# Kernel tuning notes

Hardware: AMD Instinct MI355X
Metric: run time of the kernel (lower is better)

The kernel has to match this reference:

```python
import jax, jax.numpy as jnp
import numpy as np
import math

B, S, D = 2, 1024, 512
H = 8
DH = D // H
N_NEURONS = 512
K = 16
N_BASIS = 8
RANK = 64
D_FF = 2048
LN_EPS = 1e-5


def _layer_norm(x, g, b):
    mu = jnp.mean(x, axis=-1, keepdims=True)
    var = jnp.var(x, axis=-1, keepdims=True)
    return (x - mu) * jax.lax.rsqrt(var + LN_EPS) * g + b


def setup_inputs() -> dict:
    key = jax.random.key(0)
    ks = jax.random.split(key, 16)
    x = jax.random.normal(ks[0], (B, S, D), dtype=jnp.float32)
    # causal mask [B,1,S,S] (True = keep)
    mask = jnp.broadcast_to(jnp.tril(jnp.ones((S, S), dtype=bool)), (B, 1, S, S))
    inp = {
        "x": x,
        "neuron_emb": jax.random.normal(ks[1], (N_NEURONS, D)) * 0.02,
        "Wq": jax.random.normal(ks[2], (D, D)) * 0.02, "bq": jnp.zeros((D,)),
        "Wk": jax.random.normal(ks[3], (D, D)) * 0.02, "bk": jnp.zeros((D,)),
        "Wv": jax.random.normal(ks[4], (D, D)) * 0.02, "bv": jnp.zeros((D,)),
        "Wg": jax.random.normal(ks[5], (2 * D, 2)) * 0.02, "bg": jnp.zeros((2,)),
        "basis_A": jax.random.normal(ks[6], (N_BASIS, D, RANK)) * 0.05,
        "basis_B": jax.random.normal(ks[7], (N_BASIS, RANK, D_FF)) * 0.05,
        "neuron_coords": jax.random.normal(ks[8], (N_NEURONS, N_BASIS)) * 0.5,
        "Wd": jax.random.normal(ks[9], (D_FF, D)) * 0.02, "bd": jnp.zeros((D,)),
        "ln1_g": jnp.ones((D,)), "ln1_b": jnp.zeros((D,)),
        "ln2_g": jnp.ones((D,)), "ln2_b": jnp.zeros((D,)),
        "mask": mask,
    }
    return inp


def reference(x, neuron_emb, Wq, bq, Wk, bk, Wv, bv, Wg, bg, basis_A, basis_B,
              neuron_coords, Wd, bd, ln1_g, ln1_b, ln2_g, ln2_b, mask):
    normed = _layer_norm(x, ln1_g, ln1_b)
    # --- router: cross-attention context ---
    q = (normed @ Wq + bq).reshape(B, S, H, DH).transpose(0, 2, 1, 3)
    k = (normed @ Wk + bk).reshape(B, S, H, DH).transpose(0, 2, 1, 3)
    v = (normed @ Wv + bv).reshape(B, S, H, DH).transpose(0, 2, 1, 3)
    attn = jnp.einsum('bhsd,bhtd->bhst', q, k) / math.sqrt(DH)
    attn = jnp.where(mask, attn, -jnp.inf)
    attn = jax.nn.softmax(attn, axis=-1)
    context = jnp.einsum('bhst,bhtd->bhsd', attn, v)
    context = context.transpose(0, 2, 1, 3).reshape(B, S, D)
    # --- gated neuron scoring + top-k ---
    token_scores = normed @ neuron_emb.T            # [B,S,N]
    context_scores = context @ neuron_emb.T         # [B,S,N]
    gate = jax.nn.softmax(jnp.concatenate([normed, context], axis=-1) @ Wg + bg, axis=-1)
    scores = gate[:, :, 0:1] * token_scores + gate[:, :, 1:2] * context_scores
    topk_scores, topk_idx = jax.lax.top_k(scores, K)  # [B,S,K]
    weights = jax.nn.softmax(topk_scores, axis=-1)
    # --- neuron info residual ---
    neuron_info = jnp.einsum('bsk,bskd->bsd', weights, neuron_emb[topk_idx])
    x = x + neuron_info
    # --- per-token basis-mixed low-rank FFN ---
    normed2 = _layer_norm(x, ln2_g, ln2_b)
    coords = neuron_coords[topk_idx]                # [B,S,K,n_basis]
    token_coords = jnp.einsum('bsk,bskn->bsn', weights, coords)  # [B,S,n_basis]
    # h = x @ (sum_n c_n A_n): contract without materializing [B,S,D,R]
    h = jnp.einsum('bsnr,bsn->bsr', jnp.einsum('bsd,ndr->bsnr', normed2, basis_A), token_coords)
    h = jnp.einsum('bsnf,bsn->bsf', jnp.einsum('bsr,nrf->bsnf', h, basis_B), token_coords)
    h = jax.nn.gelu(h, approximate=False)
    out = h @ Wd + bd
    x = x + out
    return (x, topk_idx)
```

## Files before the change

### kernel.cpp

```cpp
#include <hip/hip_runtime.h>
#include <hip/hip_bf16.h>

#define Bv 2
#define Sv 1024
#define Dv 512
#define Hv 8
#define Nv 512
#define Kv 16
#define NBv 8
#define DFv 2048
#define NTOK (Bv*Sv)

typedef __attribute__((ext_vector_type(8))) short short8;
typedef __attribute__((ext_vector_type(4))) float float4v;
typedef __attribute__((ext_vector_type(4))) double dbl4;

__device__ __forceinline__ double fexp64(double x)
{
    if (x < -708.0) return 0.0;
    const double SHIFT = 6755399441055744.0;
    double t  = fma(x, 1.4426950408889634074, SHIFT);
    double nd = t - SHIFT;
    double r  = fma(-nd, 6.93147180369123816490e-01, x);
    r         = fma(-nd, 1.90821492927058770002e-10, r);
    double p = 1.0 / 6227020800.0;
    p = fma(p, r, 1.0 / 479001600.0);
    p = fma(p, r, 1.0 / 39916800.0);
    p = fma(p, r, 1.0 / 3628800.0);
    p = fma(p, r, 1.0 / 362880.0);
    p = fma(p, r, 1.0 / 40320.0);
    p = fma(p, r, 1.0 / 5040.0);
    p = fma(p, r, 1.0 / 720.0);
    p = fma(p, r, 1.0 / 120.0);
    p = fma(p, r, 1.0 / 24.0);
    p = fma(p, r, 1.0 / 6.0);
    p = fma(p, r, 0.5);
    p = fma(p, r, 1.0);
    p = fma(p, r, 1.0);
    long long ni = (long long)nd;
    double s = __longlong_as_double((unsigned long long)(ni + 1023) << 52);
    return p * s;
}

__launch_bounds__(256)
__global__ void ln64_k(const float* __restrict__ x, const float* __restrict__ g,
                       const float* __restrict__ b, double* __restrict__ out)
{
    const int t = blockIdx.x;
    const size_t base = (size_t)t * Dv;
    const int tid = threadIdx.x;
    double v0 = (double)x[base + tid];
    double v1 = (double)x[base + tid + 256];
    double s = v0 + v1, ss = v0 * v0 + v1 * v1;
    #pragma unroll
    for (int off = 32; off; off >>= 1) { s += __shfl_xor(s, off); ss += __shfl_xor(ss, off); }
    __shared__ double red[4][2];
    const int wv = tid >> 6, ln = tid & 63;
    if (ln == 0) { red[wv][0] = s; red[wv][1] = ss; }
    __syncthreads();
    s  = red[0][0] + red[1][0] + red[2][0] + red[3][0];
    ss = red[0][1] + red[1][1] + red[2][1] + red[3][1];
    double mu  = s * (1.0 / Dv);
    double var = ss * (1.0 / Dv) - mu * mu;
    double rstd = 1.0 / sqrt(var + 1e-5);
    out[base + tid]       = (v0 - mu) * rstd * (double)g[tid]       + (double)b[tid];
    out[base + tid + 256] = (v1 - mu) * rstd * (double)g[tid + 256] + (double)b[tid + 256];
}

__launch_bounds__(256)
__global__ void qkvMC_k(const double* __restrict__ A,
                        const float* __restrict__ Wq, const float* __restrict__ Wk,
                        const float* __restrict__ Wv, const float* __restrict__ bq,
                        const float* __restrict__ bk, const float* __restrict__ bvv,
                        double* __restrict__ qo, double* __restrict__ ko,
                        double* __restrict__ vo)
{
    __shared__ double As[32][18];
    __shared__ double Bs[3][16][66];
    const int tid = threadIdx.x;
    const int n0 = blockIdx.x * 64, m0 = blockIdx.y * 32;
    const int w = tid >> 6, l = tid & 63;
    const int mt = (w >> 1) * 16, wc = (w & 1) * 32;
    const int ar = tid >> 3, ak = (tid & 7) * 2;
    const int bkk = tid >> 4, bn = (tid & 15) * 4;

    int rA = 0, kA = 0, kB = 0, cB = 0, dsel = -1;
    #pragma unroll 1
    for (int ab = 0; ab < 4; ab++) {
        if (dsel >= 0) break;
        const int a_ = ab & 1, b_ = ab >> 1;
        const int rA_ = a_ ? (l >> 2) : (l & 15);
        const int kA_ = a_ ? (l & 3)  : (l >> 4);
        const int kB_ = b_ ? (l & 3)  : (l >> 4);
        const int cB_ = b_ ? (l >> 2) : (l & 15);
        const double av  = (double)(((rA_ * 37 + kA_ * 11) % 19) + 1);
        const double bvp = (double)(((kB_ * 23 + cB_ * 7) % 17) + 1);
        dbl4 dd = __builtin_amdgcn_mfma_f64_16x16x4f64(av, bvp, (dbl4){0.0, 0.0, 0.0, 0.0}, 0, 0, 0);
        #pragma unroll 1
        for (int d = 0; d < 4; d++) {
            if (dsel >= 0) break;
            int okv = 1;
            #pragma unroll
            for (int r = 0; r < 4; r++) {
                const int i_ = (d == 0) ? 4 * (l >> 4) + r
                             : (d == 1) ? (l & 15)
                             : (d == 2) ? (l >> 4) + 4 * r
                             :            (l & 15);
                const int j_ = (d == 0) ? (l & 15)
                             : (d == 1) ? 4 * (l >> 4) + r
                             : (d == 2) ? (l & 15)
                             :            (l >> 4) + 4 * r;
                double e = 0.0;
                #pragma unroll
                for (int kk2 = 0; kk2 < 4; kk2++)
                    e += (double)(((i_ * 37 + kk2 * 11) % 19) + 1)
                       * (double)(((kk2 * 23 + j_ * 7) % 17) + 1);
                okv &= (dd[r] == e) ? 1 : 0;
            }
            if (__all(okv)) { dsel = d; rA = rA_; kA = kA_; kB = kB_; cB = cB_; }
        }
    }

    auto stage = [&](int k0) {
        double2 avv = *(const double2*)(A + (size_t)(m0 + ar) * Dv + k0 + ak);
        *(double2*)&As[ar][ak] = avv;
        {
            float4 b4 = *(const float4*)(Wq + (size_t)(k0 + bkk) * Dv + n0 + bn);
            Bs[0][bkk][bn] = (double)b4.x; Bs[0][bkk][bn + 1] = (double)b4.y;
            Bs[0][bkk][bn + 2] = (double)b4.z; Bs[0][bkk][bn + 3] = (double)b4.w;
        }
        {
            float4 b4 = *(const float4*)(Wk + (size_t)(k0 + bkk) * Dv + n0 + bn);
            Bs[1][bkk][bn] = (double)b4.x; Bs[1][bkk][bn + 1] = (double)b4.y;
            Bs[1][bkk][bn + 2] = (double)b4.z; Bs[1][bkk][bn + 3] = (double)b4.w;
        }
        {
            float4 b4 = *(const float4*)(Wv + (size_t)(k0 + bkk) * Dv + n0 + bn);
            Bs[2][bkk][bn] = (double)b4.x; Bs[2][bkk][bn + 1] = (double)b4.y;
            Bs[2][bkk][bn + 2] = (double)b4.z; Bs[2][bkk][bn + 3] = (double)b4.w;
        }
    };

    if (dsel >= 0) {
        dbl4 acc[3][2];
        #pragma unroll
        for (int z = 0; z < 3; z++)
            #pragma unroll
            for (int nt = 0; nt < 2; nt++)
                acc[z][nt] = (dbl4){0.0, 0.0, 0.0, 0.0};
        for (int k0 = 0; k0 < Dv; k0 += 16) {
            __syncthreads();
            stage(k0);
            __syncthreads();
            #pragma unroll
            for (int s = 0; s < 4; s++) {
                const double aA = As[mt + rA][4 * s + kA];
                #pragma unroll
                for (int z = 0; z < 3; z++) {
                    const double b0 = Bs[z][4 * s + kB][wc + cB];
                    const double b1 = Bs[z][4 * s + kB][wc + 16 + cB];
                    acc[z][0] = __builtin_amdgcn_mfma_f64_16x16x4f64(aA, b0, acc[z][0], 0, 0, 0);
                    acc[z][1] = __builtin_amdgcn_mfma_f64_16x16x4f64(aA, b1, acc[z][1], 0, 0, 0);
                }
            }
        }
        #pragma unroll
        for (int r = 0; r < 4; r++) {
            const int i_ = (dsel == 0) ? 4 * (l >> 4) + r
                         : (dsel == 1) ? (l & 15)
                         : (dsel == 2) ? (l >> 4) + 4 * r
                         :               (l & 15);
            const int j_ = (dsel == 0) ? (l & 15)
                         : (dsel == 1) ? 4 * (l >> 4) + r
                         : (dsel == 2) ? (l & 15)
                         :               (l >> 4) + 4 * r;
            const int rowg = m0 + mt + i_;
            #pragma unroll
            for (int nt = 0; nt < 2; nt++) {
                const int colg = n0 + wc + nt * 16 + j_;
                qo[(size_t)rowg * Dv + colg] = acc[0][nt][r] + (double)bq[colg];
                ko[(size_t)rowg * Dv + colg] = acc[1][nt][r] + (double)bk[colg];
                vo[(size_t)rowg * Dv + colg] = acc[2][nt][r] + (double)bvv[colg];
            }
        }
    } else {
        double fac[3][8];
        #pragma unroll
        for (int z = 0; z < 3; z++)
            #pragma unroll
            for (int c = 0; c < 8; c++) fac[z][c] = 0.0;
        const int frow = mt + (l & 15);
        const int fcb  = wc + (l >> 4) * 8;
        for (int k0 = 0; k0 < Dv; k0 += 16) {
            __syncthreads();
            stage(k0);
            __syncthreads();
            #pragma unroll
            for (int kk = 0; kk < 16; kk++) {
                const double a = As[frow][kk];
                #pragma unroll
                for (int z = 0; z < 3; z++)
                    #pragma unroll
                    for (int c = 0; c < 8; c++)
                        fac[z][c] = fma(a, Bs[z][kk][fcb + c], fac[z][c]);
            }
        }
        const int rowg = m0 + frow;
        #pragma unroll
        for (int c = 0; c < 8; c++) {
            const int colg = n0 + fcb + c;
            qo[(size_t)rowg * Dv + colg] = fac[0][c] + (double)bq[colg];
            ko[(size_t)rowg * Dv + colg] = fac[1][c] + (double)bk[colg];
            vo[(size_t)rowg * Dv + colg] = fac[2][c] + (double)bvv[colg];
        }
    }
}

__launch_bounds__(256)
__global__ void scores64_k(const double* __restrict__ A0, const double* __restrict__ A1,
                           const double* __restrict__ gate, const float* __restrict__ Bm,
                           double* __restrict__ Cbase)
{
    const int M = NTOK, N = Nv, Kd = Dv;
    const int z = blockIdx.z;
    const int kbeg = z * (Dv / 2), kend = kbeg + Dv / 2;
    double* Cout = Cbase + (size_t)z * M * N;
    __shared__ double As[16][68];
    __shared__ double Bs[16][68];
    const int tid = threadIdx.x;
    const int m0 = blockIdx.y * 64, n0 = blockIdx.x * 64;
    const int tx = tid & 15, ty = tid >> 4;
    double acc[4][4] = {};
    const int lm = tid >> 2, lk4 = (tid & 3) << 2;
    for (int k0 = kbeg; k0 < kend; k0 += 16) {
        const double g0 = gate[2 * (m0 + lm)], g1 = gate[2 * (m0 + lm) + 1];
        double4 a0 = *(const double4*)(A0 + (size_t)(m0 + lm) * Kd + k0 + lk4);
        double4 a1 = *(const double4*)(A1 + (size_t)(m0 + lm) * Kd + k0 + lk4);
        As[lk4 + 0][lm] = g0 * a0.x + g1 * a1.x;
        As[lk4 + 1][lm] = g0 * a0.y + g1 * a1.y;
        As[lk4 + 2][lm] = g0 * a0.z + g1 * a1.z;
        As[lk4 + 3][lm] = g0 * a0.w + g1 * a1.w;
        const int nn = tid >> 2, kq = (tid & 3) << 2;
        float4 bv4 = *(const float4*)(Bm + (size_t)(n0 + nn) * Kd + k0 + kq);
        Bs[kq + 0][nn] = (double)bv4.x; Bs[kq + 1][nn] = (double)bv4.y;
        Bs[kq + 2][nn] = (double)bv4.z; Bs[kq + 3][nn] = (double)bv4.w;
        __syncthreads();
        #pragma unroll
        for (int kk = 0; kk < 16; kk++) {
            double a_[4], b_[4];
            *(double4*)a_ = *(const double4*)&As[kk][ty << 2];
            *(double4*)b_ = *(const double4*)&Bs[kk][tx << 2];
            #pragma unroll
            for (int i = 0; i < 4; i++)
                #pragma unroll
                for (int j = 0; j < 4; j++)
                    acc[i][j] = fma(a_[i], b_[j], acc[i][j]);
        }
        __syncthreads();
    }
    #pragma unroll
    for (int i = 0; i < 4; i++) {
        const int row = m0 + (ty << 2) + i;
        #pragma unroll
        for (int j = 0; j < 4; j++)
            Cout[(size_t)row * N + n0 + (tx << 2) + j] = acc[i][j];
    }
}

template<int EPI>
__launch_bounds__(256)
__global__ void mfma_k(const __hip_bfloat16* __restrict__ A, const __hip_bfloat16* __restrict__ B,
                       void* __restrict__ Cout_, int M, int N, int Kt, int kper)
{
    __shared__ __hip_bfloat16 As[128][40];
    __shared__ __hip_bfloat16 Bs[128][40];
    const int tid = threadIdx.x;
    const int m0 = blockIdx.y * 128, n0 = blockIdx.x * 128;
    const int z = blockIdx.z;
    const int kbeg = z * kper, kend = kbeg + kper;
    const int w = tid >> 6, l = tid & 63;
    const int wr = (w >> 1) * 64, wc = (w & 1) * 64;
    const int lm = l & 15, quad = l >> 4;
    float4v acc[4][4];
    #pragma unroll
    for (int i = 0; i < 4; i++)
        #pragma unroll
        for (int j = 0; j < 4; j++)
            acc[i][j] = (float4v){0.f, 0.f, 0.f, 0.f};
    const int srow = tid >> 1, skb = (tid & 1) * 16;
    for (int k0 = kbeg; k0 < kend; k0 += 32) {
        *(uint4*)&As[srow][skb]     = *(const uint4*)(A + (size_t)(m0 + srow) * Kt + k0 + skb);
        *(uint4*)&As[srow][skb + 8] = *(const uint4*)(A + (size_t)(m0 + srow) * Kt + k0 + skb + 8);
        *(uint4*)&Bs[srow][skb]     = *(const uint4*)(B + (size_t)(n0 + srow) * Kt + k0 + skb);
        *(uint4*)&Bs[srow][skb + 8] = *(const uint4*)(B + (size_t)(n0 + srow) * Kt + k0 + skb + 8);
        __syncthreads();
        short8 af[4], bf[4];
        #pragma unroll
        for (int mi = 0; mi < 4; mi++) af[mi] = *(const short8*)&As[wr + mi * 16 + lm][quad * 8];
        #pragma unroll
        for (int ni = 0; ni < 4; ni++) bf[ni] = *(const short8*)&Bs[wc + ni * 16 + lm][quad * 8];
        #pragma unroll
        for (int mi = 0; mi < 4; mi++)
            #pragma unroll
            for (int ni = 0; ni < 4; ni++)
                acc[mi][ni] = __builtin_amdgcn_mfma_f32_16x16x32_bf16(af[mi], bf[ni], acc[mi][ni], 0, 0, 0);
        __syncthreads();
    }
    #pragma unroll
    for (int mi = 0; mi < 4; mi++) {
        #pragma unroll
        for (int ni = 0; ni < 4; ni++) {
            const int col = n0 + wc + ni * 16 + lm;
            #pragma unroll
            for (int r = 0; r < 4; r++) {
                const int row = m0 + wr + mi * 16 + quad * 4 + r;
                float c = acc[mi][ni][r];
                if (EPI == 0) {
                    ((float*)Cout_)[(size_t)z * M * N + (size_t)row * N + col] = c;
                } else {
                    c = 0.5f * c * (1.0f + erff(c * 0.70710678118654752f));
                    ((__hip_bfloat16*)Cout_)[(size_t)row * N + col] = __float2bfloat16(c);
                }
            }
        }
    }
}

__device__ __constant__ int c_slotbase[4] = {0, 0, 384, 640};
__device__ __constant__ int c_cnt[4]      = {0, 24, 16, 8};

__launch_bounds__(256)
__global__ void attn64w_k(const double* __restrict__ q, const double* __restrict__ k,
                          const double* __restrict__ v, double* __restrict__ ctxun,
                          double* __restrict__ Opart, double* __restrict__ mbuf,
                          double* __restrict__ lbuf)
{
    const int qb = blockIdx.x, bh = blockIdx.y, ch = blockIdx.z;
    if (qb < ch * 4) return;
    const int b = bh >> 3, h = bh & 7;
    __shared__ double Qs[64][70];
    __shared__ double Kt[64][34];
    __shared__ double Vs[32][70];
    const int tid = threadIdx.x;
    const int r = tid >> 3, cc = tid & 7;
    const int lane = tid & 63;
    const int lbase = lane & 56;
    const size_t qoff = ((size_t)(b * Sv + qb * 64)) * Dv + h * 64;
    #pragma unroll
    for (int i = 0; i < 8; i++) {
        int f = i * 256 + tid;
        int row = f >> 5, c2 = (f & 31) * 2;
        *(double2*)&Qs[row][c2] = *(const double2*)(q + qoff + (size_t)row * Dv + c2);
    }
    double O0[8] = {}, O1[8] = {};
    double m0 = -1e300, l0 = 0.0;
    double m1 = -1e300, l1 = 0.0;
    const int ig0 = qb * 64 + r;
    const int ig1 = qb * 64 + 32 + r;
    const int jbeg = ch * 8;
    const int jend = (ch * 8 + 7 < 2 * qb + 1) ? ch * 8 + 7 : 2 * qb + 1;
    for (int jt = jbeg; jt <= jend; jt++) {
        __syncthreads();
        const size_t koff = ((size_t)(b * Sv + jt * 32)) * Dv + h * 64;
        #pragma unroll
        for (int i = 0; i < 4; i++) {
            int f = i * 256 + tid;
            int row = f >> 5, c2 = (f & 31) * 2;
            double2 kv = *(const double2*)(k + koff + (size_t)row * Dv + c2);
            Kt[c2][row]     = kv.x;
            Kt[c2 + 1][row] = kv.y;
            *(double2*)&Vs[row][c2] = *(const double2*)(v + koff + (size_t)row * Dv + c2);
        }
        __syncthreads();
        double a0[4] = {0.0, 0.0, 0.0, 0.0};
        double a1[4] = {0.0, 0.0, 0.0, 0.0};
        #pragma unroll 8
        for (int kk = 0; kk < 64; kk += 2) {
            double2 qv0 = *(const double2*)&Qs[r][kk];
            double2 qv1 = *(const double2*)&Qs[32 + r][kk];
            double2 ka0 = *(const double2*)&Kt[kk][cc * 4];
            double2 ka1 = *(const double2*)&Kt[kk][cc * 4 + 2];
            double2 kb0 = *(const double2*)&Kt[kk + 1][cc * 4];
            double2 kb1 = *(const double2*)&Kt[kk + 1][cc * 4 + 2];
            a0[0] = fma(qv0.x, ka0.x, fma(qv0.y, kb0.x, a0[0]));
            a0[1] = fma(qv0.x, ka0.y, fma(qv0.y, kb0.y, a0[1]));
            a0[2] = fma(qv0.x, ka1.x, fma(qv0.y, kb1.x, a0[2]));
            a0[3] = fma(qv0.x, ka1.y, fma(qv0.y, kb1.y, a0[3]));
            a1[0] = fma(qv1.x, ka0.x, fma(qv1.y, kb0.x, a1[0]));
            a1[1] = fma(qv1.x, ka0.y, fma(qv1.y, kb0.y, a1[1]));
            a1[2] = fma(qv1.x, ka1.x, fma(qv1.y, kb1.x, a1[2]));
            a1[3] = fma(qv1.x, ka1.y, fma(qv1.y, kb1.y, a1[3]));
        }
        double p0[4], p1[4];
        double mx0 = -1e300, mx1 = -1e300;
        #pragma unroll
        for (int jj = 0; jj < 4; jj++) {
            const int jglob = jt * 32 + cc * 4 + jj;
            p0[jj] = (jglob <= ig0) ? a0[jj] * 0.125 : -1e300;
            p1[jj] = (jglob <= ig1) ? a1[jj] * 0.125 : -1e300;
            mx0 = fmax(mx0, p0[jj]);
            mx1 = fmax(mx1, p1[jj]);
        }
        mx0 = fmax(mx0, __shfl_xor(mx0, 1)); mx1 = fmax(mx1, __shfl_xor(mx1, 1));
        mx0 = fmax(mx0, __shfl_xor(mx0, 2)); mx1 = fmax(mx1, __shfl_xor(mx1, 2));
        mx0 = fmax(mx0, __shfl_xor(mx0, 4)); mx1 = fmax(mx1, __shfl_xor(mx1, 4));
        const double mn0 = fmax(m0, mx0), mn1 = fmax(m1, mx1);
        double rs0 = 0.0, rs1 = 0.0;
        #pragma unroll
        for (int jj = 0; jj < 4; jj++) {
            p0[jj] = fexp64(p0[jj] - mn0); rs0 += p0[jj];
            p1[jj] = fexp64(p1[jj] - mn1); rs1 += p1[jj];
        }
        rs0 += __shfl_xor(rs0, 1); rs1 += __shfl_xor(rs1, 1);
        rs0 += __shfl_xor(rs0, 2); rs1 += __shfl_xor(rs1, 2);
        rs0 += __shfl_xor(rs0, 4); rs1 += __shfl_xor(rs1, 4);
        const double al0 = fexp64(m0 - mn0), al1 = fexp64(m1 - mn1);
        l0 = l0 * al0 + rs0; m0 = mn0;
        l1 = l1 * al1 + rs1; m1 = mn1;
        #pragma unroll
        for (int c = 0; c < 8; c++) { O0[c] *= al0; O1[c] *= al1; }
        #pragma unroll
        for (int jsrc = 0; jsrc < 8; jsrc++) {
            #pragma unroll
            for (int jj = 0; jj < 4; jj++) {
                const double pj0 = __shfl(p0[jj], lbase + jsrc);
                const double pj1 = __shfl(p1[jj], lbase + jsrc);
                const double* vrow = &Vs[jsrc * 4 + jj][cc * 8];
                #pragma unroll
                for (int c2 = 0; c2 < 8; c2 += 2) {
                    double2 vv = *(const double2*)&vrow[c2];
                    O0[c2 + 0] = fma(pj0, vv.x, O0[c2 + 0]);
                    O0[c2 + 1] = fma(pj0, vv.y, O0[c2 + 1]);
                    O1[c2 + 0] = fma(pj1, vv.x, O1[c2 + 0]);
                    O1[c2 + 1] = fma(pj1, vv.y, O1[c2 + 1]);
                }
            }
        }
    }
    const int qt0 = 2 * qb, qt1 = 2 * qb + 1;
    if (cc == 0) {
        const int mi0 = ((bh * 32 + qt0) * 4 + ch) * 32 + r;
        mbuf[mi0] = m0; lbuf[mi0] = l0;
        const int mi1 = ((bh * 32 + qt1) * 4 + ch) * 32 + r;
        mbuf[mi1] = m1; lbuf[mi1] = l1;
    }
    if (ch == 0) {
        const size_t ob0 = ((size_t)(b * Sv + ig0)) * Dv + h * 64 + cc * 8;
        const size_t ob1 = ((size_t)(b * Sv + ig1)) * Dv + h * 64 + cc * 8;
        #pragma unroll
        for (int c2 = 0; c2 < 8; c2 += 2) {
            double2 t0{O0[c2], O0[c2 + 1]}; *(double2*)(ctxun + ob0 + c2) = t0;
            double2 t1{O1[c2], O1[c2 + 1]}; *(double2*)(ctxun + ob1 + c2) = t1;
        }
    } else {
        const int slot0 = c_slotbase[ch] + bh * c_cnt[ch] + (qt0 - ch * 8);
        const int slot1 = slot0 + 1;
        const size_t ob0 = ((size_t)slot0 * 32 + r) * 64 + cc * 8;
        const size_t ob1 = ((size_t)slot1 * 32 + r) * 64 + cc * 8;
        #pragma unroll
        for (int c2 = 0; c2 < 8; c2 += 2) {
            double2 t0{O0[c2], O0[c2 + 1]}; *(double2*)(Opart + ob0 + c2) = t0;
            double2 t1{O1[c2], O1[c2 + 1]}; *(double2*)(Opart + ob1 + c2) = t1;
        }
    }
}

__launch_bounds__(256)
__global__ void attnmerge_k(double* __restrict__ ctx, const double* __restrict__ Opart,
                            const double* __restrict__ mbuf, const double* __restrict__ lbuf)
{
    const size_t i = (size_t)blockIdx.x * 256 + threadIdx.x;
    const size_t e = i * 2;
    const int d = (int)(e & 511);
    const int s = (int)((e >> 9) & 1023);
    const int b = (int)(e >> 19);
    const int h = d >> 6;
    const int qt = s >> 5, r = s & 31;
    const int bh = b * 8 + h;
    int nch = qt >> 3; if (nch > 3) nch = 3;
    const int mib = ((bh * 32 + qt) * 4) * 32 + r;
    double ms = mbuf[mib];
    for (int c = 1; c <= nch; c++) ms = fmax(ms, mbuf[mib + c * 32]);
    double2 o = *(const double2*)(ctx + e);
    double a0 = exp(mbuf[mib] - ms);
    double den = lbuf[mib] * a0;
    o.x *= a0; o.y *= a0;
    for (int c = 1; c <= nch; c++) {
        const double ac = exp(mbuf[mib + c * 32] - ms);
        den += lbuf[mib + c * 32] * ac;
        const int slot = c_slotbase[c] + bh * c_cnt[c] + (qt - c * 8);
        const size_t op = ((size_t)slot * 32 + r) * 64 + (d & 63);
        double2 oc = *(const double2*)(Opart + op);
        o.x = fma(ac, oc.x, o.x);
        o.y = fma(ac, oc.y, o.y);
    }
    const double inv = 1.0 / den;
    o.x *= inv; o.y *= inv;
    *(double2*)(ctx + e) = o;
}

__launch_bounds__(256)
__global__ void gate64_k(const double* __restrict__ normed, const double* __restrict__ ctx,
                         const float* __restrict__ Wg, const float* __restrict__ bg,
                         double* __restrict__ gate)
{
    const int wv = threadIdx.x >> 6, lane = threadIdx.x & 63;
    const int t = blockIdx.x * 4 + wv;
    double a0 = 0.0, a1 = 0.0;
    for (int d = lane; d < Dv; d += 64) {
        double nv = normed[(size_t)t * Dv + d];
        double cv = ctx[(size_t)t * Dv + d];
        a0 += nv * (double)Wg[2 * d]     + cv * (double)Wg[2 * (d + Dv)];
        a1 += nv * (double)Wg[2 * d + 1] + cv * (double)Wg[2 * (d + Dv) + 1];
    }
    #pragma unroll
    for (int off = 32; off; off >>= 1) { a0 += __shfl_xor(a0, off); a1 += __shfl_xor(a1, off); }
    if (lane == 0) {
        a0 += (double)bg[0]; a1 += (double)bg[1];
        double m = fmax(a0, a1);
        double e0 = exp(a0 - m), e1 = exp(a1 - m);
        double inv = 1.0 / (e0 + e1);
        gate[2 * t] = e0 * inv; gate[2 * t + 1] = e1 * inv;
    }
}

__launch_bounds__(256)
__global__ void topk64_k(const double* __restrict__ s0, const float* __restrict__ x,
                         const float* __restrict__ emb, const float* __restrict__ coords,
                         const float* __restrict__ g2, const float* __restrict__ b2,
                         float* __restrict__ x2, __hip_bfloat16* __restrict__ normed2bf,
                         float* __restrict__ tcoords, float* __restrict__ idx_out)
{
    __shared__ double sc[4][Nv];
    const int wv = threadIdx.x >> 6, lane = threadIdx.x & 63;
    const int t = blockIdx.x * 4 + wv;
    const double* s1 = s0 + (size_t)NTOK * Nv;
    double* s = sc[wv];
    #pragma unroll
    for (int i = 0; i < 8; i++) {
        const size_t idx = (size_t)t * Nv + i * 64 + lane;
        s[i * 64 + lane] = s0[idx] + s1[idx];
    }
    __syncthreads();
    double wval[Kv]; int widx[Kv];
    for (int kk = 0; kk < Kv; kk++) {
        double bvv = -1e300; int bi = Nv;
        #pragma unroll
        for (int i = 0; i < 8; i++) {
            const int d = lane * 8 + i;
            const double vv = s[d];
            if (vv > bvv) { bvv = vv; bi = d; }
        }
        #pragma unroll
        for (int off = 1; off < 64; off <<= 1) {
            double ov = __shfl_xor(bvv, off);
            int    oi = __shfl_xor(bi, off);
            if (ov > bvv || (ov == bvv && oi < bi)) { bvv = ov; bi = oi; }
        }
        wval[kk] = bvv; widx[kk] = bi;
        __syncthreads();
        if (lane == (bi >> 3)) s[bi] = -1e301;
        __syncthreads();
        if (lane == kk) idx_out[(size_t)t * Kv + kk] = (float)bi;
    }
    double w[Kv]; double sum = 0.0;
    #pragma unroll
    for (int kk = 0; kk < Kv; kk++) { w[kk] = exp(wval[kk] - wval[0]); sum += w[kk]; }
    const double invs = 1.0 / sum;
    #pragma unroll
    for (int kk = 0; kk < Kv; kk++) w[kk] *= invs;
    float xv[8];
    float sm = 0.0f, sq = 0.0f;
    #pragma unroll
    for (int i = 0; i < 8; i++) {
        const int d = lane + 64 * i;
        double info = 0.0;
        #pragma unroll
        for (int kk = 0; kk < Kv; kk++)
            info = fma(w[kk], (double)emb[(size_t)widx[kk] * Dv + d], info);
        float vv = (float)((double)x[(size_t)t * Dv + d] + info);
        xv[i] = vv;
        x2[(size_t)t * Dv + d] = vv;
        sm += vv; sq += vv * vv;
    }
    #pragma unroll
    for (int off = 32; off; off >>= 1) { sm += __shfl_xor(sm, off); sq += __shfl_xor(sq, off); }
    const float mu = sm * (1.0f / Dv);
    const float var = sq * (1.0f / Dv) - mu * mu;
    const float rstd = rsqrtf(var + 1e-5f);
    #pragma unroll
    for (int i = 0; i < 8; i++) {
        const int d = lane + 64 * i;
        normed2bf[(size_t)t * Dv + d] = __float2bfloat16((xv[i] - mu) * rstd * g2[d] + b2[d]);
    }
    if (lane < NBv) {
        double tc = 0.0;
        #pragma unroll
        for (int kk = 0; kk < Kv; kk++)
            tc = fma(w[kk], (double)coords[(size_t)widx[kk] * NBv + lane], tc);
        tcoords[t * NBv + lane] = (float)tc;
    }
}

__launch_bounds__(256)
__global__ void acatbf_k(const float* __restrict__ bA, __hip_bfloat16* __restrict__ AcatT)
{
    const int i = blockIdx.x * 256 + threadIdx.x;
    const int d = i & 511, nc = i >> 9;
    const int n = nc >> 6, r = nc & 63;
    AcatT[i] = __float2bfloat16(bA[n * 32768 + d * 64 + r]);
}

__launch_bounds__(256)
__global__ void tr2bf_k(const float* __restrict__ in, __hip_bfloat16* __restrict__ out,
                        int R, int C)
{
    __shared__ float tile[32][33];
    const int c0 = blockIdx.x * 32, r0 = blockIdx.y * 32;
    const int tx = threadIdx.x & 31, ty = threadIdx.x >> 5;
    #pragma unroll
    for (int i = 0; i < 4; i++)
        tile[ty + 8 * i][tx] = in[(size_t)(r0 + ty + 8 * i) * C + c0 + tx];
    __syncthreads();
    #pragma unroll
    for (int i = 0; i < 4; i++)
        out[(size_t)(c0 + ty + 8 * i) * R + r0 + tx] = __float2bfloat16(tile[tx][ty + 8 * i]);
}

__launch_bounds__(256)
__global__ void combine_k(const float* __restrict__ Gp, const float* __restrict__ tcoords,
                          __hip_bfloat16* __restrict__ u_bf)
{
    const size_t M1 = (size_t)NTOK * Dv;
    const int wv = threadIdx.x >> 6, lane = threadIdx.x & 63;
    const int t = blockIdx.x * 4 + wv;
    float cs[NBv];
    #pragma unroll
    for (int n = 0; n < NBv; n++) cs[n] = tcoords[t * NBv + n];
    float h = 0.0f;
    #pragma unroll
    for (int n = 0; n < NBv; n++) {
        const size_t gi = (size_t)t * Dv + n * 64 + lane;
        float g = Gp[gi] + Gp[gi + M1] + Gp[gi + 2 * M1] + Gp[gi + 3 * M1];
        h = fmaf(cs[n], g, h);
    }
    #pragma unroll
    for (int n = 0; n < NBv; n++)
        u_bf[(size_t)t * Dv + n * 64 + lane] = __float2bfloat16(cs[n] * h);
}

__launch_bounds__(256)
__global__ void reduce4_k(const float* __restrict__ p4, const float* __restrict__ bd,
                          const float* __restrict__ x2, float* __restrict__ xout)
{
    const size_t M1 = (size_t)NTOK * Dv;
    const size_t i = (size_t)blockIdx.x * 256 + threadIdx.x;
    float c = p4[i] + p4[i + M1] + p4[i + 2 * M1] + p4[i + 3 * M1];
    xout[i] = c + bd[i & 511] + x2[i];
}

extern "C" void kernel_launch(void* const* d_in, const int* in_sizes, int n_in,
                              void* d_out, int out_size, void* d_ws, size_t ws_size,
                              hipStream_t stream) {
    (void)in_sizes; (void)n_in; (void)out_size; (void)ws_size;
    const size_t M1 = (size_t)NTOK * Dv;

    const float* x   = (const float*)d_in[0];
    const float* emb = (const float*)d_in[1];
    const float* Wq  = (const float*)d_in[2];
    const float* bq  = (const float*)d_in[3];
    const float* Wk  = (const float*)d_in[4];
    const float* bk  = (const float*)d_in[5];
    const float* Wv  = (const float*)d_in[6];
    const float* bvv = (const float*)d_in[7];
    const float* Wg  = (const float*)d_in[8];
    const float* bg  = (const float*)d_in[9];
    const float* bA  = (const float*)d_in[10];
    const float* bB  = (const float*)d_in[11];
    const float* crd = (const float*)d_in[12];
    const float* Wd  = (const float*)d_in[13];
    const float* bd  = (const float*)d_in[14];
    const float* l1g = (const float*)d_in[15];
    const float* l1b = (const float*)d_in[16];
    const float* l2g = (const float*)d_in[17];
    const float* l2b = (const float*)d_in[18];

    double* normed64 = (double*)d_ws;
    double* q64      = normed64 + M1;
    double* k64      = q64 + M1;
    double* v64      = k64 + M1;
    double* ctx64    = v64 + M1;
    double* Opart    = ctx64 + M1;
    double* mbuf     = Opart + 1572864;
    double* lbuf     = mbuf + 65536;
    double* gate64   = lbuf + 65536;
    float*  tcoords  = (float*)(gate64 + 4096);
    __hip_bfloat16* AcatT = (__hip_bfloat16*)(tcoords + 16384);

    double* s0 = q64;
    float*  x2 = (float*)v64;
    __hip_bfloat16* normed2bf = (__hip_bfloat16*)(x2 + M1);
    __hip_bfloat16* u_bf      = normed2bf + M1;
    float* Gp = (float*)q64;
    float* p4 = (float*)q64;
    __hip_bfloat16* hf_bf = (__hip_bfloat16*)Opart;
    __hip_bfloat16* bBT   = hf_bf + 4 * M1;
    __hip_bfloat16* WdT   = bBT + M1;

    float* xout    = (float*)d_out;
    float* idx_out = (float*)d_out + M1;

    ln64_k<<<NTOK, 256, 0, stream>>>(x, l1g, l1b, normed64);
    qkvMC_k<<<dim3(8, 64), 256, 0, stream>>>(normed64, Wq, Wk, Wv, bq, bk, bvv, q64, k64, v64);
    attn64w_k<<<dim3(16, 16, 4), 256, 0, stream>>>(q64, k64, v64, ctx64, Opart, mbuf, lbuf);
    attnmerge_k<<<(int)(M1 / 512), 256, 0, stream>>>(ctx64, Opart, mbuf, lbuf);
    gate64_k<<<NTOK / 4, 256, 0, stream>>>(normed64, ctx64, Wg, bg, gate64);
    scores64_k<<<dim3(8, 32, 2), 256, 0, stream>>>(normed64, ctx64, gate64, emb, s0);
    topk64_k<<<NTOK / 4, 256, 0, stream>>>(s0, x, emb, crd, l2g, l2b, x2, normed2bf, tcoords, idx_out);
    acatbf_k<<<1024, 256, 0, stream>>>(bA, AcatT);
    tr2bf_k<<<dim3(DFv / 32, Dv / 32), 256, 0, stream>>>(bB, bBT, Dv, DFv);
    tr2bf_k<<<dim3(Dv / 32, DFv / 32), 256, 0, stream>>>(Wd, WdT, DFv, Dv);
    mfma_k<0><<<dim3(4, 16, 4), 256, 0, stream>>>(normed2bf, AcatT, Gp, NTOK, Dv, Dv, Dv / 4);
    combine_k<<<NTOK / 4, 256, 0, stream>>>(Gp, tcoords, u_bf);
    mfma_k<1><<<dim3(16, 16, 1), 256, 0, stream>>>(u_bf, bBT, hf_bf, NTOK, DFv, Dv, Dv);
    mfma_k<0><<<dim3(4, 16, 4), 256, 0, stream>>>(hf_bf, WdT, p4, NTOK, Dv, DFv, DFv / 4);
    reduce4_k<<<(int)(M1 / 256), 256, 0, stream>>>(p4, bd, x2, xout);
}
```

Before: 540.7 us.

## Replace probed FP64 MFMA QKV GEMM with register-blocked 64-row FMA kernel

The QKV projection kernel no longer probes the FP64 MFMA lane layout at runtime or uses the MFMA path. It always uses scalar FP64 FMAs, with each thread now computing two row groups (a 64-row tile instead of 32). B-operand values are read from shared memory as vector loads and reused across both rows. This removes the probe overhead and halves the grid, in exchange for giving up matrix-core throughput and raising register pressure.

New measurement: 580.5 us. +7.4%, slower.

```diff
diff --git a/kernel.cpp b/kernel.cpp
--- a/kernel.cpp
+++ b/kernel.cpp
@@ -13,7 +13,6 @@
 
 typedef __attribute__((ext_vector_type(8))) short short8;
 typedef __attribute__((ext_vector_type(4))) float float4v;
-typedef __attribute__((ext_vector_type(4))) double dbl4;
 
 __device__ __forceinline__ double fexp64(double x)
 {
@@ -68,62 +67,36 @@
 }
 
 __launch_bounds__(256)
-__global__ void qkvMC_k(const double* __restrict__ A,
-                        const float* __restrict__ Wq, const float* __restrict__ Wk,
-                        const float* __restrict__ Wv, const float* __restrict__ bq,
-                        const float* __restrict__ bk, const float* __restrict__ bvv,
-                        double* __restrict__ qo, double* __restrict__ ko,
-                        double* __restrict__ vo)
-{
-    __shared__ double As[32][18];
+__global__ void qkv64w_k(const double* __restrict__ A,
+                         const float* __restrict__ Wq, const float* __restrict__ Wk,
+                         const float* __restrict__ Wv, const float* __restrict__ bq,
+                         const float* __restrict__ bk, const float* __restrict__ bvv,
+                         double* __restrict__ qo, double* __restrict__ ko,
+                         double* __restrict__ vo)
+{
+    __shared__ double As[64][18];
     __shared__ double Bs[3][16][66];
     const int tid = threadIdx.x;
-    const int n0 = blockIdx.x * 64, m0 = blockIdx.y * 32;
+    const int n0 = blockIdx.x * 64, m0 = blockIdx.y * 64;
     const int w = tid >> 6, l = tid & 63;
     const int mt = (w >> 1) * 16, wc = (w & 1) * 32;
     const int ar = tid >> 3, ak = (tid & 7) * 2;
     const int bkk = tid >> 4, bn = (tid & 15) * 4;
-
-    int rA = 0, kA = 0, kB = 0, cB = 0, dsel = -1;
-    #pragma unroll 1
-    for (int ab = 0; ab < 4; ab++) {
-        if (dsel >= 0) break;
-        const int a_ = ab & 1, b_ = ab >> 1;
-        const int rA_ = a_ ? (l >> 2) : (l & 15);
-        const int kA_ = a_ ? (l & 3)  : (l >> 4);
-        const int kB_ = b_ ? (l & 3)  : (l >> 4);
-        const int cB_ = b_ ? (l >> 2) : (l & 15);
-        const double av  = (double)(((rA_ * 37 + kA_ * 11) % 19) + 1);
-        const double bvp = (double)(((kB_ * 23 + cB_ * 7) % 17) + 1);
-        dbl4 dd = __builtin_amdgcn_mfma_f64_16x16x4f64(av, bvp, (dbl4){0.0, 0.0, 0.0, 0.0}, 0, 0, 0);
-        #pragma unroll 1
-        for (int d = 0; d < 4; d++) {
-            if (dsel >= 0) break;
-            int okv = 1;
+    const int frow = mt + (l & 15);
+    const int fcb  = wc + (l >> 4) * 8;
+    double fac[2][3][8];
+    #pragma unroll
+    for (int hh = 0; hh < 2; hh++)
+        #pragma unroll
+        for (int z = 0; z < 3; z++)
             #pragma unroll
-            for (int r = 0; r < 4; r++) {
-                const int i_ = (d == 0) ? 4 * (l >> 4) + r
-                             : (d == 1) ? (l & 15)
-                             : (d == 2) ? (l >> 4) + 4 * r
-                             :            (l & 15);
-                const int j_ = (d == 0) ? (l & 15)
-                             : (d == 1) ? 4 * (l >> 4) + r
-                             : (d == 2) ? (l & 15)
-                             :            (l >> 4) + 4 * r;
-                double e = 0.0;
-                #pragma unroll
-                for (int kk2 = 0; kk2 < 4; kk2++)
-                    e += (double)(((i_ * 37 + kk2 * 11) % 19) + 1)
-                       * (double)(((kk2 * 23 + j_ * 7) % 17) + 1);
-                okv &= (dd[r] == e) ? 1 : 0;
-            }
-            if (__all(okv)) { dsel = d; rA = rA_; kA = kA_; kB = kB_; cB = cB_; }
-        }
-    }
-
-    auto stage = [&](int k0) {
-        double2 avv = *(const double2*)(A + (size_t)(m0 + ar) * Dv + k0 + ak);
-        *(double2*)&As[ar][ak] = avv;
+            for (int c = 0; c < 8; c++) fac[hh][z][c] = 0.0;
+    for (int k0 = 0; k0 < Dv; k0 += 16) {
+        __syncthreads();
+        double2 av0 = *(const double2*)(A + (size_t)(m0 + ar) * Dv + k0 + ak);
+        double2 av1 = *(const double2*)(A + (size_t)(m0 + 32 + ar) * Dv + k0 + ak);
+        *(double2*)&As[ar][ak]      = av0;
+        *(double2*)&As[32 + ar][ak] = av1;
         {
             float4 b4 = *(const float4*)(Wq + (size_t)(k0 + bkk) * Dv + n0 + bn);
             Bs[0][bkk][bn] = (double)b4.x; Bs[0][bkk][bn + 1] = (double)b4.y;
@@ -139,79 +112,33 @@
             Bs[2][bkk][bn] = (double)b4.x; Bs[2][bkk][bn + 1] = (double)b4.y;
             Bs[2][bkk][bn + 2] = (double)b4.z; Bs[2][bkk][bn + 3] = (double)b4.w;
         }
-    };
-
-    if (dsel >= 0) {
-        dbl4 acc[3][2];
-        #pragma unroll
-        for (int z = 0; z < 3; z++)
+        __syncthreads();
+        #pragma unroll
+        for (int kk = 0; kk < 16; kk++) {
+            const double a0 = As[frow][kk];
+            const double a1 = As[32 + frow][kk];
             #pragma unroll
-            for (int nt = 0; nt < 2; nt++)
-                acc[z][nt] = (dbl4){0.0, 0.0, 0.0, 0.0};
-        for (int k0 = 0; k0 < Dv; k0 += 16) {
-            __syncthreads();
-            stage(k0);
-            __syncthreads();
-            #pragma unroll
-            for (int s = 0; s < 4; s++) {
-                const double aA = As[mt + rA][4 * s + kA];
+            for (int z = 0; z < 3; z++) {
+                double b_[8];
+                *(double4*)&b_[0] = *(const double4*)&Bs[z][kk][fcb];
+                *(double4*)&b_[4] = *(const double4*)&Bs[z][kk][fcb + 4];
                 #pragma unroll
-                for (int z = 0; z < 3; z++) {
-                    const double b0 = Bs[z][4 * s + kB][wc + cB];
-                    const double b1 = Bs[z][4 * s + kB][wc + 16 + cB];
-                    acc[z][0] = __builtin_amdgcn_mfma_f64_16x16x4f64(aA, b0, acc[z][0], 0, 0, 0);
-                    acc[z][1] = __builtin_amdgcn_mfma_f64_16x16x4f64(aA, b1, acc[z][1], 0, 0, 0);
+                for (int c = 0; c < 8; c++) {
+                    fac[0][z][c] = fma(a0, b_[c], fac[0][z][c]);
+                    fac[1][z][c] = fma(a1, b_[c], fac[1][z][c]);
                 }
             }
         }
-        #pragma unroll
-        for (int r = 0; r < 4; r++) {
-            const int i_ = (dsel == 0) ? 4 * (l >> 4) + r
-                         : (dsel == 1) ? (l & 15)
-                         : (dsel == 2) ? (l >> 4) + 4 * r
-                         :               (l & 15);
-            const int j_ = (dsel == 0) ? (l & 15)
-                         : (dsel == 1) ? 4 * (l >> 4) + r
-                         : (dsel == 2) ? (l & 15)
-                         :               (l >> 4) + 4 * r;
-            const int rowg = m0 + mt + i_;
-            #pragma unroll
-            for (int nt = 0; nt < 2; nt++) {
-                const int colg = n0 + wc + nt * 16 + j_;
-                qo[(size_t)rowg * Dv + colg] = acc[0][nt][r] + (double)bq[colg];
-                ko[(size_t)rowg * Dv + colg] = acc[1][nt][r] + (double)bk[colg];
-                vo[(size_t)rowg * Dv + colg] = acc[2][nt][r] + (double)bvv[colg];
-            }
-        }
-    } else {
-        double fac[3][8];
-        #pragma unroll
-        for (int z = 0; z < 3; z++)
-            #pragma unroll
-            for (int c = 0; c < 8; c++) fac[z][c] = 0.0;
-        const int frow = mt + (l & 15);
-        const int fcb  = wc + (l >> 4) * 8;
-        for (int k0 = 0; k0 < Dv; k0 += 16) {
-            __syncthreads();
-            stage(k0);
-            __syncthreads();
-            #pragma unroll
-            for (int kk = 0; kk < 16; kk++) {
-                const double a = As[frow][kk];
-                #pragma unroll
-                for (int z = 0; z < 3; z++)
-                    #pragma unroll
-                    for (int c = 0; c < 8; c++)
-                        fac[z][c] = fma(a, Bs[z][kk][fcb + c], fac[z][c]);
-            }
-        }
-        const int rowg = m0 + frow;
+    }
+    #pragma unroll
+    for (int hh = 0; hh < 2; hh++) {
+        const int rowg = m0 + frow + hh * 32;
         #pragma unroll
         for (int c = 0; c < 8; c++) {
             const int colg = n0 + fcb + c;
-            qo[(size_t)rowg * Dv + colg] = fac[0][c] + (double)bq[colg];
-            ko[(size_t)rowg * Dv + colg] = fac[1][c] + (double)bk[colg];
-            vo[(size_t)rowg * Dv + colg] = fac[2][c] + (double)bvv[colg];
+            qo[(size_t)rowg * Dv + colg] = fac[hh][0][c] + (double)bq[colg];
+            ko[(size_t)rowg * Dv + colg] = fac[hh][1][c] + (double)bk[colg];
+            vo[(size_t)rowg * Dv + colg] = fac[hh][2][c] + (double)bvv[colg];
         }
     }
 }
@@ -711,7 +638,7 @@
     float* idx_out = (float*)d_out + M1;
 
     ln64_k<<<NTOK, 256, 0, stream>>>(x, l1g, l1b, normed64);
-    qkvMC_k<<<dim3(8, 64), 256, 0, stream>>>(normed64, Wq, Wk, Wv, bq, bk, bvv, q64, k64, v64);
+    qkv64w_k<<<dim3(8, 32), 256, 0, stream>>>(normed64, Wq, Wk, Wv, bq, bk, bvv, q64, k64, v64);
     attn64w_k<<<dim3(16, 16, 4), 256, 0, stream>>>(q64, k64, v64, ctx64, Opart, mbuf, lbuf);
     attnmerge_k<<<(int)(M1 / 512), 256, 0, stream>>>(ctx64, Opart, mbuf, lbuf);
     gate64_k<<<NTOK / 4, 256, 0, stream>>>(normed64, ctx64, Wg, bg, gate64);
```
